# Performance work log

Measured on AMD Instinct MI355X. Metric: run time of the kernel, lower is better.

The kernel has to match this reference:

```python
import jax, jax.numpy as jnp
import numpy as np

NUM_HEADS = 12

def setup_inputs() -> dict:
    key = jax.random.key(0)
    ks = jax.random.split(key, 5)
    dim = 768
    x = jax.random.normal(ks[0], (2, 64, 64, dim), dtype=jnp.float32)
    qkv_w = jax.random.normal(ks[1], (3 * dim, dim), dtype=jnp.float32) * 0.02
    qkv_b = jax.random.normal(ks[2], (3 * dim,), dtype=jnp.float32) * 0.02
    proj_w = jax.random.normal(ks[3], (dim, dim), dtype=jnp.float32) * 0.02
    proj_b = jax.random.normal(ks[4], (dim,), dtype=jnp.float32) * 0.02
    return {"x": x, "qkv_w": qkv_w, "qkv_b": qkv_b, "proj_w": proj_w, "proj_b": proj_b}

def reference(x, qkv_w, qkv_b, proj_w, proj_b):
    B, H, W, C = x.shape
    N = H * W
    nh = NUM_HEADS
    hd = C // nh
    scale = hd ** -0.5
    # qkv linear: (B,H,W,3C)
    qkv = jnp.einsum('bhwc,dc->bhwd', x, qkv_w) + qkv_b
    qkv = qkv.reshape(B, N, 3, nh, hd).transpose(2, 0, 3, 1, 4)  # (3,B,nh,N,hd)
    q, k, v = qkv[0], qkv[1], qkv[2]
    # (B,nh,N,N) attention scores, stable softmax
    attn = jax.nn.softmax(jnp.einsum('bhqd,bhkd->bhqk', q * scale, k), axis=-1)
    out = jnp.einsum('bhqk,bhkd->bhqd', attn, v)  # (B,nh,N,hd)
    out = out.transpose(0, 2, 1, 3).reshape(B, N, C)
    # Source quirk: for 4D input the output stays (B, N, C) after proj.
    return jnp.einsum('bnc,dc->bnd', out, proj_w) + proj_b
```

## Files before the change

### kernel.cpp

```cpp
#include <hip/hip_runtime.h>
#include <hip/hip_bf16.h>

#define LOG2E 1.44269504088896340736f

typedef __attribute__((ext_vector_type(8))) short short8;
typedef __attribute__((ext_vector_type(4))) float f32x4;

__device__ __forceinline__ unsigned short f2bf(float f) {
    unsigned int u = __float_as_uint(f);
    u += 0x7fffu + ((u >> 16) & 1u);
    return (unsigned short)(u >> 16);
}

__device__ __forceinline__ unsigned cvt_pk_bf16(float a, float b) {
    unsigned r;
    asm("v_cvt_pk_bf16_f32 %0, %1, %2" : "=v"(r) : "v"(a), "v"(b));
    return r;
}

__device__ __forceinline__ float fast_exp2(float x) {
    float r;
    asm("v_exp_f32 %0, %1" : "=v"(r) : "v"(x));
    return r;
}

__global__ void cvt_f32_to_bf16(const float* __restrict__ in,
                                unsigned short* __restrict__ out, int n4) {
    int stride = gridDim.x * blockDim.x;
    for (int i = blockIdx.x * blockDim.x + threadIdx.x; i < n4; i += stride) {
        float4 v = ((const float4*)in)[i];
        ushort4 o;
        o.x = f2bf(v.x); o.y = f2bf(v.y); o.z = f2bf(v.z); o.w = f2bf(v.w);
        ((ushort4*)out)[i] = o;
    }
}

template <int EPI>
__global__ __launch_bounds__(256, 2)
void gemm_bt(const unsigned short* __restrict__ A,
             const unsigned short* __restrict__ B,
             const float* __restrict__ bias,
             void* __restrict__ Cout,
             int M, int N, int K) {
    __shared__ unsigned short As[128][72];
    __shared__ unsigned short Bs[128][72];

    const int tid  = threadIdx.x;
    const int wave = tid >> 6, lane = tid & 63;
    const int fr = lane & 15, fg = lane >> 4;
    const int wm = (wave >> 1) * 64, wn = (wave & 1) * 64;
    const int m0 = blockIdx.y * 128, n0 = blockIdx.x * 128;
    const int trow = tid >> 3, tseg = tid & 7;

    f32x4 acc[4][4];
#pragma unroll
    for (int m = 0; m < 4; m++)
#pragma unroll
        for (int n = 0; n < 4; n++) acc[m][n] = (f32x4){0.f, 0.f, 0.f, 0.f};

    short8 rA[4], rB[4];
#pragma unroll
    for (int c = 0; c < 4; c++) {
        int r = trow + c * 32;
        rA[c] = *(const short8*)(A + (size_t)(m0 + r) * K + tseg * 8);
        rB[c] = *(const short8*)(B + (size_t)(n0 + r) * K + tseg * 8);
    }

    for (int k0 = 0; k0 < K; k0 += 64) {
        __syncthreads();
#pragma unroll
        for (int c = 0; c < 4; c++) {
            int r = trow + c * 32;
            *(short8*)&As[r][tseg * 8] = rA[c];
            *(short8*)&Bs[r][tseg * 8] = rB[c];
        }
        if (k0 + 64 < K) {
#pragma unroll
            for (int c = 0; c < 4; c++) {
                int r = trow + c * 32;
                rA[c] = *(const short8*)(A + (size_t)(m0 + r) * K + k0 + 64 + tseg * 8);
                rB[c] = *(const short8*)(B + (size_t)(n0 + r) * K + k0 + 64 + tseg * 8);
            }
        }
        __syncthreads();
#pragma unroll
        for (int ks = 0; ks < 2; ks++) {
            short8 af[4], bfr[4];
#pragma unroll
            for (int m = 0; m < 4; m++)
                af[m] = *(const short8*)&As[wm + m * 16 + fr][ks * 32 + fg * 8];
#pragma unroll
            for (int n = 0; n < 4; n++)
                bfr[n] = *(const short8*)&Bs[wn + n * 16 + fr][ks * 32 + fg * 8];
#pragma unroll
            for (int m = 0; m < 4; m++)
#pragma unroll
                for (int n = 0; n < 4; n++)
                    acc[m][n] = __builtin_amdgcn_mfma_f32_16x16x32_bf16(
                        af[m], bfr[n], acc[m][n], 0, 0, 0);
        }
    }

#pragma unroll
    for (int m = 0; m < 4; m++) {
#pragma unroll
        for (int n = 0; n < 4; n++) {
            int gn = n0 + wn + n * 16 + fr;
            float bv = bias[gn];
#pragma unroll
            for (int j = 0; j < 4; j++) {
                int gm = m0 + wm + m * 16 + fg * 4 + j;
                float v = acc[m][n][j] + bv;
                if (EPI == 0) {
                    int which = gn / 768, rem = gn % 768;
                    int h = rem >> 6, d = rem & 63;
                    int b = gm >> 12, nn = gm & 4095;
                    if (which == 0) v *= (0.125f * LOG2E);
                    unsigned short* o = (unsigned short*)Cout;
                    size_t base = (((size_t)which * 2 + b) * 12 + h) * 262144;
                    if (which == 2) {
                        int k6 = nn & 63;
                        int kp = (k6 & 0x23) | ((k6 & 0x08) << 1) |
                                 ((k6 & 0x04) << 1) | ((k6 & 0x10) >> 2);
                        o[base + (size_t)d * 4096 + (nn & ~63) + kp] = f2bf(v);
                    } else {
                        o[base + (size_t)nn * 64 + d] = f2bf(v);
                    }
                } else {
                    float* o = (float*)Cout;
                    o[(size_t)gm * 768 + gn] = v;
                }
            }
        }
    }
}

__global__ __launch_bounds__(256, 2)
void attn_fwd(const unsigned short* __restrict__ qkv,
              unsigned short* __restrict__ outp) {
    __shared__ unsigned short Ks[64][72];
    __shared__ unsigned short Vt[64][72];

    const int tid  = threadIdx.x;
    const int wave = tid >> 6, lane = tid & 63;
    const int fr = lane & 15, fg = lane >> 4;
    const int frp = (fr & 3) | ((fr & 4) << 1) | ((fr & 8) >> 1);
    const int fgl = fg & 1, fgh = fg >> 1;

    const int qt = blockIdx.x;
    const int bh = blockIdx.y;
    const int b = bh / 12, h = bh % 12;

    const size_t headsz = (size_t)4096 * 64;
    const unsigned short* qh  = qkv + ((size_t)b * 12 + h) * headsz;
    const unsigned short* kh  = qkv + ((size_t)(2 + b) * 12 + h) * headsz;
    const unsigned short* vht = qkv + ((size_t)(4 + b) * 12 + h) * headsz;

    const int qw = qt * 128 + wave * 32;

    short8 qf[2][2];
#pragma unroll
    for (int qm = 0; qm < 2; qm++)
#pragma unroll
        for (int ks = 0; ks < 2; ks++)
            qf[qm][ks] = *(const short8*)(qh + (size_t)(qw + qm * 16 + fr) * 64 +
                                          ks * 32 + fg * 8);

    float mrow[2] = {-1e30f, -1e30f}, lrow[2] = {0.f, 0.f};
    f32x4 accO[4][2];
#pragma unroll
    for (int df = 0; df < 4; df++)
#pragma unroll
        for (int qm = 0; qm < 2; qm++) accO[df][qm] = (f32x4){0.f, 0.f, 0.f, 0.f};

    const int r = tid >> 3, sg = tid & 7;

    short8 rK[2], rV[2];
#pragma unroll
    for (int c = 0; c < 2; c++) {
        int kr = r + c * 32;
        rK[c] = *(const short8*)(kh + (size_t)kr * 64 + sg * 8);
        rV[c] = *(const short8*)(vht + (size_t)kr * 4096 + sg * 8);
    }

    for (int kt = 0; kt < 64; kt++) {
        __syncthreads();
#pragma unroll
        for (int c = 0; c < 2; c++) {
            int kr = r + c * 32;
            *(short8*)&Ks[kr][sg * 8] = rK[c];
            *(short8*)&Vt[kr][sg * 8] = rV[c];
        }
        if (kt < 63) {
            const unsigned short* kb = kh + (size_t)(kt + 1) * 4096;
#pragma unroll
            for (int c = 0; c < 2; c++) {
                int kr = r + c * 32;
                rK[c] = *(const short8*)(kb + kr * 64 + sg * 8);
                rV[c] = *(const short8*)(vht + (size_t)kr * 4096 + (kt + 1) * 64 + sg * 8);
            }
        }
        __syncthreads();

        f32x4 s[4][2];
#pragma unroll
        for (int nf = 0; nf < 4; nf++)
#pragma unroll
            for (int qm = 0; qm < 2; qm++) s[nf][qm] = (f32x4){0.f, 0.f, 0.f, 0.f};
        __builtin_amdgcn_s_setprio(1);
#pragma unroll
        for (int ks = 0; ks < 2; ks++) {
            short8 kf[4];
#pragma unroll
            for (int nf = 0; nf < 4; nf++)
                kf[nf] = *(const short8*)&Ks[nf * 16 + frp][ks * 32 + fg * 8];
#pragma unroll
            for (int nf = 0; nf < 4; nf++)
#pragma unroll
                for (int qm = 0; qm < 2; qm++)
                    s[nf][qm] = __builtin_amdgcn_mfma_f32_16x16x32_bf16(
                        kf[nf], qf[qm][ks], s[nf][qm], 0, 0, 0);
        }
        __builtin_amdgcn_s_setprio(0);

        unsigned P2[2][4][2];
#pragma unroll
        for (int qm = 0; qm < 2; qm++) {
            float mx = s[0][qm][0];
#pragma unroll
            for (int nf = 0; nf < 4; nf++)
#pragma unroll
                for (int j = 0; j < 4; j++)
                    if (nf | j) mx = fmaxf(mx, s[nf][qm][j]);
            mx = fmaxf(mx, __shfl_xor(mx, 16));
            mx = fmaxf(mx, __shfl_xor(mx, 32));
            if (__all(mx - mrow[qm] <= 8.0f)) {
                float rs = 0.f;
#pragma unroll
                for (int nf = 0; nf < 4; nf++)
#pragma unroll
                    for (int j = 0; j < 4; j++) {
                        float p = fast_exp2(s[nf][qm][j] - mrow[qm]);
                        s[nf][qm][j] = p;
                        rs += p;
                    }
                rs += __shfl_xor(rs, 16);
                rs += __shfl_xor(rs, 32);
                lrow[qm] += rs;
            } else {
                float mnew = fmaxf(mrow[qm], mx);
                float corr = fast_exp2(mrow[qm] - mnew);
                mrow[qm] = mnew;
                float rs = 0.f;
#pragma unroll
                for (int nf = 0; nf < 4; nf++)
#pragma unroll
                    for (int j = 0; j < 4; j++) {
                        float p = fast_exp2(s[nf][qm][j] - mnew);
                        s[nf][qm][j] = p;
                        rs += p;
                    }
                rs += __shfl_xor(rs, 16);
                rs += __shfl_xor(rs, 32);
                lrow[qm] = lrow[qm] * corr + rs;
#pragma unroll
                for (int df = 0; df < 4; df++) accO[df][qm] *= corr;
            }
#pragma unroll
            for (int nf = 0; nf < 4; nf++) {
                P2[qm][nf][0] = cvt_pk_bf16(s[nf][qm][0], s[nf][qm][1]);
                P2[qm][nf][1] = cvt_pk_bf16(s[nf][qm][2], s[nf][qm][3]);
            }
        }

        __builtin_amdgcn_s_setprio(1);
#pragma unroll
        for (int ks = 0; ks < 2; ks++) {
            short8 pf[2];
#pragma unroll
            for (int qm = 0; qm < 2; qm++) {
                union { unsigned w[4]; short8 v; } u;
                u.w[0] = P2[qm][2 * ks][0];     u.w[1] = P2[qm][2 * ks][1];
                u.w[2] = P2[qm][2 * ks + 1][0]; u.w[3] = P2[qm][2 * ks + 1][1];
                pf[qm] = u.v;
            }
#pragma unroll
            for (int df = 0; df < 4; df++) {
                short8 vf = *(const short8*)&Vt[df * 16 + fr][ks * 32 + fgl * 16 + fgh * 8];
#pragma unroll
                for (int qm = 0; qm < 2; qm++)
                    accO[df][qm] = __builtin_amdgcn_mfma_f32_16x16x32_bf16(
                        vf, pf[qm], accO[df][qm], 0, 0, 0);
            }
        }
        __builtin_amdgcn_s_setprio(0);
    }

#pragma unroll
    for (int qm = 0; qm < 2; qm++) {
        float inv = 1.0f / lrow[qm];
        int gq = qw + qm * 16 + fr;
        size_t rowoff = (size_t)(b * 4096 + gq) * 768 + h * 64;
#pragma unroll
        for (int df = 0; df < 4; df++) {
            ushort4 o;
            o.x = f2bf(accO[df][qm][0] * inv);
            o.y = f2bf(accO[df][qm][1] * inv);
            o.z = f2bf(accO[df][qm][2] * inv);
            o.w = f2bf(accO[df][qm][3] * inv);
            *(ushort4*)(outp + rowoff + df * 16 + fg * 4) = o;
        }
    }
}

extern "C" void kernel_launch(void* const* d_in, const int* in_sizes, int n_in,
                              void* d_out, int out_size, void* d_ws, size_t ws_size,
                              hipStream_t stream) {
    const float* x      = (const float*)d_in[0];
    const float* qkv_w  = (const float*)d_in[1];
    const float* qkv_b  = (const float*)d_in[2];
    const float* proj_w = (const float*)d_in[3];
    const float* proj_b = (const float*)d_in[4];
    float* out = (float*)d_out;

    char* ws = (char*)d_ws;
    unsigned short* x_bf    = (unsigned short*)(ws);
    unsigned short* w1_bf   = (unsigned short*)(ws + 12582912);
    unsigned short* w2_bf   = (unsigned short*)(ws + 16121856);
    unsigned short* qkv_sep = (unsigned short*)(ws + 17301504);
    unsigned short* att     = (unsigned short*)(ws + 55050240);

    cvt_f32_to_bf16<<<2048, 256, 0, stream>>>(x,      x_bf,  6291456 / 4);
    cvt_f32_to_bf16<<<1024, 256, 0, stream>>>(qkv_w,  w1_bf, 1769472 / 4);
    cvt_f32_to_bf16<<<576,  256, 0, stream>>>(proj_w, w2_bf,  589824 / 4);

    gemm_bt<0><<<dim3(18, 64), 256, 0, stream>>>(x_bf, w1_bf, qkv_b, qkv_sep,
                                                 8192, 2304, 768);

    attn_fwd<<<dim3(32, 24), 256, 0, stream>>>(qkv_sep, att);

    gemm_bt<1><<<dim3(6, 64), 256, 0, stream>>>(att, w2_bf, proj_b, out,
                                                8192, 768, 768);
}
```

Before: 236.6 us.

## Switch attention MFMAs to 32x32x16 tiles with per-lane row softmax

Replaces the 16x16x32 bf16 MFMA tiling in the attention kernel with 32x32x16 MFMAs, so each lane owns a single query row. The row max and row sum become mostly in-register reductions needing one cross-lane shuffle instead of two. The V-transpose layout in the QKV epilogue drops its within-block key permutation to match the new P fragment layout. The aim is fewer MFMA issues and less softmax shuffle and bookkeeping work, at the cost of larger accumulators and possibly different LDS bank-conflict behaviour.

```diff
diff --git a/kernel.cpp b/kernel.cpp
--- a/kernel.cpp
+++ b/kernel.cpp
@@ -5,6 +5,7 @@
 
 typedef __attribute__((ext_vector_type(8))) short short8;
 typedef __attribute__((ext_vector_type(4))) float f32x4;
+typedef __attribute__((ext_vector_type(16))) float f32x16;
 
 __device__ __forceinline__ unsigned short f2bf(float f) {
     unsigned int u = __float_as_uint(f);
@@ -118,14 +119,10 @@
                     if (which == 0) v *= (0.125f * LOG2E);
                     unsigned short* o = (unsigned short*)Cout;
                     size_t base = (((size_t)which * 2 + b) * 12 + h) * 262144;
-                    if (which == 2) {
-                        int k6 = nn & 63;
-                        int kp = (k6 & 0x23) | ((k6 & 0x08) << 1) |
-                                 ((k6 & 0x04) << 1) | ((k6 & 0x10) >> 2);
-                        o[base + (size_t)d * 4096 + (nn & ~63) + kp] = f2bf(v);
-                    } else {
+                    if (which == 2)
+                        o[base + (size_t)d * 4096 + nn] = f2bf(v);
+                    else
                         o[base + (size_t)nn * 64 + d] = f2bf(v);
-                    }
                 } else {
                     float* o = (float*)Cout;
                     o[(size_t)gm * 768 + gn] = v;
@@ -143,9 +140,8 @@
 
     const int tid  = threadIdx.x;
     const int wave = tid >> 6, lane = tid & 63;
-    const int fr = lane & 15, fg = lane >> 4;
-    const int frp = (fr & 3) | ((fr & 4) << 1) | ((fr & 8) >> 1);
-    const int fgl = fg & 1, fgh = fg >> 1;
+    const int l31 = lane & 31, hh = lane >> 5;
+    const int l31p = (l31 & 0x13) | ((l31 & 4) << 1) | ((l31 & 8) >> 1);
 
     const int qt = blockIdx.x;
     const int bh = blockIdx.y;
@@ -157,21 +153,15 @@
     const unsigned short* vht = qkv + ((size_t)(4 + b) * 12 + h) * headsz;
 
     const int qw = qt * 128 + wave * 32;
-
-    short8 qf[2][2];
-#pragma unroll
-    for (int qm = 0; qm < 2; qm++)
-#pragma unroll
-        for (int ks = 0; ks < 2; ks++)
-            qf[qm][ks] = *(const short8*)(qh + (size_t)(qw + qm * 16 + fr) * 64 +
-                                          ks * 32 + fg * 8);
-
-    float mrow[2] = {-1e30f, -1e30f}, lrow[2] = {0.f, 0.f};
-    f32x4 accO[4][2];
-#pragma unroll
-    for (int df = 0; df < 4; df++)
-#pragma unroll
-        for (int qm = 0; qm < 2; qm++) accO[df][qm] = (f32x4){0.f, 0.f, 0.f, 0.f};
+    const int gq = qw + l31;
+
+    short8 qf[4];
+#pragma unroll
+    for (int ks = 0; ks < 4; ks++)
+        qf[ks] = *(const short8*)(qh + (size_t)gq * 64 + ks * 16 + hh * 8);
+
+    float mrow = -1e30f, lrow = 0.f;
+    f32x16 accA = (f32x16)0.f, accB = (f32x16)0.f;
 
     const int r = tid >> 3, sg = tid & 7;
 
@@ -202,114 +192,96 @@
         }
         __syncthreads();
 
-        f32x4 s[4][2];
-#pragma unroll
-        for (int nf = 0; nf < 4; nf++)
-#pragma unroll
-            for (int qm = 0; qm < 2; qm++) s[nf][qm] = (f32x4){0.f, 0.f, 0.f, 0.f};
+        f32x16 s0 = (f32x16)0.f, s1 = (f32x16)0.f;
         __builtin_amdgcn_s_setprio(1);
 #pragma unroll
-        for (int ks = 0; ks < 2; ks++) {
-            short8 kf[4];
-#pragma unroll
-            for (int nf = 0; nf < 4; nf++)
-                kf[nf] = *(const short8*)&Ks[nf * 16 + frp][ks * 32 + fg * 8];
-#pragma unroll
-            for (int nf = 0; nf < 4; nf++)
-#pragma unroll
-                for (int qm = 0; qm < 2; qm++)
-                    s[nf][qm] = __builtin_amdgcn_mfma_f32_16x16x32_bf16(
-                        kf[nf], qf[qm][ks], s[nf][qm], 0, 0, 0);
+        for (int ks = 0; ks < 4; ks++) {
+            short8 kf0 = *(const short8*)&Ks[l31p][ks * 16 + hh * 8];
+            short8 kf1 = *(const short8*)&Ks[32 + l31p][ks * 16 + hh * 8];
+            s0 = __builtin_amdgcn_mfma_f32_32x32x16_bf16(kf0, qf[ks], s0, 0, 0, 0);
+            s1 = __builtin_amdgcn_mfma_f32_32x32x16_bf16(kf1, qf[ks], s1, 0, 0, 0);
         }
         __builtin_amdgcn_s_setprio(0);
 
-        unsigned P2[2][4][2];
-#pragma unroll
-        for (int qm = 0; qm < 2; qm++) {
-            float mx = s[0][qm][0];
-#pragma unroll
-            for (int nf = 0; nf < 4; nf++)
-#pragma unroll
-                for (int j = 0; j < 4; j++)
-                    if (nf | j) mx = fmaxf(mx, s[nf][qm][j]);
-            mx = fmaxf(mx, __shfl_xor(mx, 16));
-            mx = fmaxf(mx, __shfl_xor(mx, 32));
-            if (__all(mx - mrow[qm] <= 8.0f)) {
-                float rs = 0.f;
-#pragma unroll
-                for (int nf = 0; nf < 4; nf++)
-#pragma unroll
-                    for (int j = 0; j < 4; j++) {
-                        float p = fast_exp2(s[nf][qm][j] - mrow[qm]);
-                        s[nf][qm][j] = p;
-                        rs += p;
-                    }
-                rs += __shfl_xor(rs, 16);
-                rs += __shfl_xor(rs, 32);
-                lrow[qm] += rs;
-            } else {
-                float mnew = fmaxf(mrow[qm], mx);
-                float corr = fast_exp2(mrow[qm] - mnew);
-                mrow[qm] = mnew;
-                float rs = 0.f;
-#pragma unroll
-                for (int nf = 0; nf < 4; nf++)
-#pragma unroll
-                    for (int j = 0; j < 4; j++) {
-                        float p = fast_exp2(s[nf][qm][j] - mnew);
-                        s[nf][qm][j] = p;
-                        rs += p;
-                    }
-                rs += __shfl_xor(rs, 16);
-                rs += __shfl_xor(rs, 32);
-                lrow[qm] = lrow[qm] * corr + rs;
-#pragma unroll
-                for (int df = 0; df < 4; df++) accO[df][qm] *= corr;
-            }
-#pragma unroll
-            for (int nf = 0; nf < 4; nf++) {
-                P2[qm][nf][0] = cvt_pk_bf16(s[nf][qm][0], s[nf][qm][1]);
-                P2[qm][nf][1] = cvt_pk_bf16(s[nf][qm][2], s[nf][qm][3]);
-            }
+        float t[16];
+#pragma unroll
+        for (int i = 0; i < 8; i++) t[i] = fmaxf(s0[2 * i], s0[2 * i + 1]);
+#pragma unroll
+        for (int i = 0; i < 8; i++) t[i + 8] = fmaxf(s1[2 * i], s1[2 * i + 1]);
+#pragma unroll
+        for (int w = 8; w; w >>= 1)
+#pragma unroll
+            for (int i = 0; i < 8; i++)
+                if (i < w) t[i] = fmaxf(t[i], t[i + w]);
+        float mx = fmaxf(t[0], __shfl_xor(t[0], 32));
+
+        if (!__all(mx - mrow <= 8.0f)) {
+            float mnew = fmaxf(mrow, mx);
+            float corr = fast_exp2(mrow - mnew);
+            mrow = mnew;
+            lrow *= corr;
+#pragma unroll
+            for (int i = 0; i < 16; i++) { accA[i] *= corr; accB[i] *= corr; }
+        }
+#pragma unroll
+        for (int i = 0; i < 16; i++) {
+            s0[i] = fast_exp2(s0[i] - mrow);
+            s1[i] = fast_exp2(s1[i] - mrow);
+        }
+#pragma unroll
+        for (int i = 0; i < 8; i++) t[i] = s0[2 * i] + s0[2 * i + 1];
+#pragma unroll
+        for (int i = 0; i < 8; i++) t[i + 8] = s1[2 * i] + s1[2 * i + 1];
+#pragma unroll
+        for (int w = 8; w; w >>= 1)
+#pragma unroll
+            for (int i = 0; i < 8; i++)
+                if (i < w) t[i] += t[i + w];
+        lrow += t[0] + __shfl_xor(t[0], 32);
+
+        short8 pf[4];
+        {
+            union { unsigned w[4]; short8 v; } up;
+            up.w[0] = cvt_pk_bf16(s0[0], s0[1]);  up.w[1] = cvt_pk_bf16(s0[2], s0[3]);
+            up.w[2] = cvt_pk_bf16(s0[4], s0[5]);  up.w[3] = cvt_pk_bf16(s0[6], s0[7]);
+            pf[0] = up.v;
+            up.w[0] = cvt_pk_bf16(s0[8], s0[9]);  up.w[1] = cvt_pk_bf16(s0[10], s0[11]);
+            up.w[2] = cvt_pk_bf16(s0[12], s0[13]); up.w[3] = cvt_pk_bf16(s0[14], s0[15]);
+            pf[1] = up.v;
+            up.w[0] = cvt_pk_bf16(s1[0], s1[1]);  up.w[1] = cvt_pk_bf16(s1[2], s1[3]);
+            up.w[2] = cvt_pk_bf16(s1[4], s1[5]);  up.w[3] = cvt_pk_bf16(s1[6], s1[7]);
+            pf[2] = up.v;
+            up.w[0] = cvt_pk_bf16(s1[8], s1[9]);  up.w[1] = cvt_pk_bf16(s1[10], s1[11]);
+            up.w[2] = cvt_pk_bf16(s1[12], s1[13]); up.w[3] = cvt_pk_bf16(s1[14], s1[15]);
+            pf[3] = up.v;
         }
 
         __builtin_amdgcn_s_setprio(1);
 #pragma unroll
-        for (int ks = 0; ks < 2; ks++) {
-            short8 pf[2];
-#pragma unroll
-            for (int qm = 0; qm < 2; qm++) {
-                union { unsigned w[4]; short8 v; } u;
-                u.w[0] = P2[qm][2 * ks][0];     u.w[1] = P2[qm][2 * ks][1];
-                u.w[2] = P2[qm][2 * ks + 1][0]; u.w[3] = P2[qm][2 * ks + 1][1];
-                pf[qm] = u.v;
-            }
-#pragma unroll
-            for (int df = 0; df < 4; df++) {
-                short8 vf = *(const short8*)&Vt[df * 16 + fr][ks * 32 + fgl * 16 + fgh * 8];
-#pragma unroll
-                for (int qm = 0; qm < 2; qm++)
-                    accO[df][qm] = __builtin_amdgcn_mfma_f32_16x16x32_bf16(
-                        vf, pf[qm], accO[df][qm], 0, 0, 0);
-            }
+        for (int ks2 = 0; ks2 < 4; ks2++) {
+            short8 vf0 = *(const short8*)&Vt[l31][ks2 * 16 + hh * 8];
+            short8 vf1 = *(const short8*)&Vt[32 + l31][ks2 * 16 + hh * 8];
+            accA = __builtin_amdgcn_mfma_f32_32x32x16_bf16(vf0, pf[ks2], accA, 0, 0, 0);
+            accB = __builtin_amdgcn_mfma_f32_32x32x16_bf16(vf1, pf[ks2], accB, 0, 0, 0);
         }
         __builtin_amdgcn_s_setprio(0);
     }
 
-#pragma unroll
-    for (int qm = 0; qm < 2; qm++) {
-        float inv = 1.0f / lrow[qm];
-        int gq = qw + qm * 16 + fr;
-        size_t rowoff = (size_t)(b * 4096 + gq) * 768 + h * 64;
-#pragma unroll
-        for (int df = 0; df < 4; df++) {
-            ushort4 o;
-            o.x = f2bf(accO[df][qm][0] * inv);
-            o.y = f2bf(accO[df][qm][1] * inv);
-            o.z = f2bf(accO[df][qm][2] * inv);
-            o.w = f2bf(accO[df][qm][3] * inv);
-            *(ushort4*)(outp + rowoff + df * 16 + fg * 4) = o;
-        }
+    float inv = 1.0f / lrow;
+    size_t rowoff = (size_t)(b * 4096 + gq) * 768 + h * 64;
+#pragma unroll
+    for (int g = 0; g < 4; g++) {
+        ushort4 o;
+        o.x = f2bf(accA[4 * g + 0] * inv);
+        o.y = f2bf(accA[4 * g + 1] * inv);
+        o.z = f2bf(accA[4 * g + 2] * inv);
+        o.w = f2bf(accA[4 * g + 3] * inv);
+        *(ushort4*)(outp + rowoff + g * 8 + hh * 4) = o;
+        o.x = f2bf(accB[4 * g + 0] * inv);
+        o.y = f2bf(accB[4 * g + 1] * inv);
+        o.z = f2bf(accB[4 * g + 2] * inv);
+        o.w = f2bf(accB[4 * g + 3] * inv);
+        *(ushort4*)(outp + rowoff + 32 + g * 8 + hh * 4) = o;
     }
 }
 
```

Result: faster. 226.3 us (-4.4%).
